# Performance work log

Hardware: AMD Instinct MI355X
Metric: run time of the kernel (lower is better)

## Reference

```python
import jax, jax.numpy as jnp
import numpy as np

NEG_SLOPE = 0.2  # LeakyReLU slope used by default activation_attn


def setup_inputs() -> dict:
    key = jax.random.key(0)
    k1, k2, k3, k4, k5 = jax.random.split(key, 5)
    N, K, F, H, D = 50000, 16, 128, 8, 64
    s = 1.0 / np.sqrt(F)  # roughly torch Linear init scale
    return {
        "x_self": jax.random.normal(k1, (N, F), dtype=jnp.float32),
        "x_neigh": jax.random.normal(k2, (N, K, F), dtype=jnp.float32),
        "W": jax.random.normal(k3, (H, F, D), dtype=jnp.float32) * s,
        "a_self": jax.random.normal(k4, (H, F), dtype=jnp.float32) * s,
        "a_neigh": jax.random.normal(k5, (H, F), dtype=jnp.float32) * s,
    }


def reference(x_self, x_neigh, W, a_self, a_neigh):
    # x_self: [N, F], x_neigh: [N, K, F]
    # x_all = concat(self, neigh) along neighbor axis -> [N, K+1, F]
    x_all = jnp.concatenate([x_self[:, None, :], x_neigh], axis=1)
    # per-head attention logits (each head's fc_attn_* is Linear(F, 1), no bias)
    logit_self = jnp.einsum('nf,hf->nh', x_self, a_self)          # [N, H]
    logit_all = jnp.einsum('nkf,hf->nkh', x_all, a_neigh)         # [N, K+1, H]
    logits = logit_self[:, None, :] + logit_all                   # [N, K+1, H]
    logits = jnp.where(logits >= 0, logits, NEG_SLOPE * logits)   # LeakyReLU(0.2)
    attn = jax.nn.softmax(logits, axis=1)                         # softmax over neighbors
    # per-head projection of all nodes: Linear(F, D), no bias
    xw = jnp.einsum('nkf,hfd->nkhd', x_all, W)                    # [N, K+1, H, D]
    h = jnp.einsum('nkhd,nkh->nhd', xw, attn)                     # [N, H, D]
    N, H, D = h.shape
    # concat aggregation: heads stacked along feature dim (head 0 first)
    return h.reshape(N, H * D)
```

## Files before the change

### kernel.cpp

```cpp
#include <hip/hip_runtime.h>

#define NTHREADS 256
#define NB 4
#define K 16
#define KP1 17
#define F 128
#define H 8
#define D 64
#define FP 132
#define NEG_SLOPE 0.2f


__global__ __launch_bounds__(NTHREADS, 4) void gat_kernel(
    const float* __restrict__ x_self,
    const float* __restrict__ x_neigh,
    const float* __restrict__ W,
    const float* __restrict__ a_self,
    const float* __restrict__ a_neigh,
    float* __restrict__ out,
    int N)
{
    __shared__ __align__(16) float xall[NB][KP1][FP];
    __shared__ __align__(16) float attn[NB][KP1][H];
    __shared__ float self_s[NB][H];

    float* yb = (float*)xall;

    const int tid = threadIdx.x;
    const int node0 = blockIdx.x * NB;

    {
        const int tot_self = NB * (F / 4);
        for (int i = tid; i < tot_self; i += NTHREADS) {
            int nb = i / (F / 4);
            int f4 = i % (F / 4);
            if (node0 + nb < N) {
                float4 v = ((const float4*)(x_self + (size_t)(node0 + nb) * F))[f4];
                *(float4*)&xall[nb][0][f4 * 4] = v;
            }
        }
        const int tot_n = NB * K * (F / 4);
        for (int i = tid; i < tot_n; i += NTHREADS) {
            int nb  = i / (K * F / 4);
            int rem = i % (K * F / 4);
            int k   = rem / (F / 4);
            int f4  = rem % (F / 4);
            if (node0 + nb < N) {
                float4 v = ((const float4*)(x_neigh + ((size_t)(node0 + nb) * K + k) * F))[f4];
                *(float4*)&xall[nb][k + 1][f4 * 4] = v;
            }
        }
    }
    __syncthreads();

    {
        const int p  = tid & 7;
        const int h  = (tid >> 3) & 7;
        const int nb = tid >> 6;
        const float* av  = a_neigh + h * F;
        const float* xr0 = &xall[nb][2 * p][0];
        const float* xr1 = &xall[nb][2 * p + 1][0];
        float4 s0 = {0.f, 0.f, 0.f, 0.f}, s1 = s0;
        #pragma unroll 8
        for (int f4 = 0; f4 < F / 4; f4++) {
            float4 avv = ((const float4*)av)[f4];
            float4 x0 = *(const float4*)(xr0 + f4 * 4);
            float4 x1 = *(const float4*)(xr1 + f4 * 4);
            s0.x += x0.x * avv.x; s0.y += x0.y * avv.y;
            s0.z += x0.z * avv.z; s0.w += x0.w * avv.w;
            s1.x += x1.x * avv.x; s1.y += x1.y * avv.y;
            s1.z += x1.z * avv.z; s1.w += x1.w * avv.w;
        }
        attn[nb][2 * p][h]     = (s0.x + s0.y) + (s0.z + s0.w);
        attn[nb][2 * p + 1][h] = (s1.x + s1.y) + (s1.z + s1.w);

        if (tid < 32) {
            const int h2  = tid & 7;
            const int nb2 = tid >> 3;
            const float* avn = a_neigh + h2 * F;
            const float* avs = a_self  + h2 * F;
            const float* x16 = &xall[nb2][16][0];
            const float* xs  = &xall[nb2][0][0];
            float4 t0 = {0.f, 0.f, 0.f, 0.f}, t1 = t0;
            #pragma unroll 8
            for (int f4 = 0; f4 < F / 4; f4++) {
                float4 an = ((const float4*)avn)[f4];
                float4 as = ((const float4*)avs)[f4];
                float4 v0 = *(const float4*)(x16 + f4 * 4);
                float4 v1 = *(const float4*)(xs  + f4 * 4);
                t0.x += v0.x * an.x; t0.y += v0.y * an.y;
                t0.z += v0.z * an.z; t0.w += v0.w * an.w;
                t1.x += v1.x * as.x; t1.y += v1.y * as.y;
                t1.z += v1.z * as.z; t1.w += v1.w * as.w;
            }
            attn[nb2][16][h2] = (t0.x + t0.y) + (t0.z + t0.w);
            self_s[nb2][h2]   = (t1.x + t1.y) + (t1.z + t1.w);
        }
    }
    __syncthreads();

    for (int i = tid; i < NB * H; i += NTHREADS) {
        int nb = i >> 3, h = i & 7;
        float sl = self_s[nb][h];
        float m = -1e30f;
        #pragma unroll
        for (int k = 0; k < KP1; k++) {
            float lg = sl + attn[nb][k][h];
            lg = (lg >= 0.f) ? lg : NEG_SLOPE * lg;
            attn[nb][k][h] = lg;
            m = fmaxf(m, lg);
        }
        float s = 0.f;
        #pragma unroll
        for (int k = 0; k < KP1; k++) {
            float e = __expf(attn[nb][k][h] - m);
            attn[nb][k][h] = e;
            s += e;
        }
        float inv = 1.0f / s;
        #pragma unroll
        for (int k = 0; k < KP1; k++) attn[nb][k][h] *= inv;
    }
    __syncthreads();

    {
        const int h  = (tid >> 5) & 7;
        const int f4 = tid & 31;
        float4 acc[NB];
        #pragma unroll
        for (int j = 0; j < NB; j++) acc[j] = {0.f, 0.f, 0.f, 0.f};
        for (int k = 0; k < KP1; k++) {
            #pragma unroll
            for (int j = 0; j < NB; j++) {
                float a = attn[j][k][h];
                float4 xv = *(const float4*)&xall[j][k][f4 * 4];
                acc[j].x += a * xv.x; acc[j].y += a * xv.y;
                acc[j].z += a * xv.z; acc[j].w += a * xv.w;
            }
        }
        __syncthreads();
        #pragma unroll
        for (int j = 0; j < NB; j++) {
            *(float4*)&yb[((size_t)j * H + h) * F + f4 * 4] = acc[j];
        }
    }
    __syncthreads();

    {
        const int lane = tid & 63;
        const int w    = tid >> 6;
        const int fg   = lane >> 4;
        const int d4   = lane & 15;
        const int h0 = w, h1 = w + 4;
        const float* Wb0 = W + ((size_t)h0 * F) * D + d4 * 4;
        const float* Wb1 = W + ((size_t)h1 * F) * D + d4 * 4;

        float4 acc0[NB], acc1[NB];
        #pragma unroll
        for (int nb = 0; nb < NB; nb++) {
            acc0[nb] = {0.f, 0.f, 0.f, 0.f};
            acc1[nb] = {0.f, 0.f, 0.f, 0.f};
        }

        for (int fb = 0; fb < 8; fb++) {
            const int f0 = fb * 16 + fg * 4;
            float4 w0[4], w1[4];
            #pragma unroll
            for (int ff = 0; ff < 4; ff++) {
                w0[ff] = *(const float4*)(Wb0 + (size_t)(f0 + ff) * D);
                w1[ff] = *(const float4*)(Wb1 + (size_t)(f0 + ff) * D);
            }
            float4 y0[NB], y1[NB];
            #pragma unroll
            for (int nb = 0; nb < NB; nb++) {
                y0[nb] = *(const float4*)&yb[((size_t)nb * H + h0) * F + f0];
                y1[nb] = *(const float4*)&yb[((size_t)nb * H + h1) * F + f0];
            }
            #pragma unroll
            for (int nb = 0; nb < NB; nb++) {
                acc0[nb].x += y0[nb].x * w0[0].x + y0[nb].y * w0[1].x + y0[nb].z * w0[2].x + y0[nb].w * w0[3].x;
                acc0[nb].y += y0[nb].x * w0[0].y + y0[nb].y * w0[1].y + y0[nb].z * w0[2].y + y0[nb].w * w0[3].y;
                acc0[nb].z += y0[nb].x * w0[0].z + y0[nb].y * w0[1].z + y0[nb].z * w0[2].z + y0[nb].w * w0[3].z;
                acc0[nb].w += y0[nb].x * w0[0].w + y0[nb].y * w0[1].w + y0[nb].z * w0[2].w + y0[nb].w * w0[3].w;
                acc1[nb].x += y1[nb].x * w1[0].x + y1[nb].y * w1[1].x + y1[nb].z * w1[2].x + y1[nb].w * w1[3].x;
                acc1[nb].y += y1[nb].x * w1[0].y + y1[nb].y * w1[1].y + y1[nb].z * w1[2].y + y1[nb].w * w1[3].y;
                acc1[nb].z += y1[nb].x * w1[0].z + y1[nb].y * w1[1].z + y1[nb].z * w1[2].z + y1[nb].w * w1[3].z;
                acc1[nb].w += y1[nb].x * w1[0].w + y1[nb].y * w1[1].w + y1[nb].z * w1[2].w + y1[nb].w * w1[3].w;
            }
        }

        #pragma unroll
        for (int nb = 0; nb < NB; nb++) {
            acc0[nb].x += __shfl_xor(acc0[nb].x, 16); acc0[nb].x += __shfl_xor(acc0[nb].x, 32);
            acc0[nb].y += __shfl_xor(acc0[nb].y, 16); acc0[nb].y += __shfl_xor(acc0[nb].y, 32);
            acc0[nb].z += __shfl_xor(acc0[nb].z, 16); acc0[nb].z += __shfl_xor(acc0[nb].z, 32);
            acc0[nb].w += __shfl_xor(acc0[nb].w, 16); acc0[nb].w += __shfl_xor(acc0[nb].w, 32);
            acc1[nb].x += __shfl_xor(acc1[nb].x, 16); acc1[nb].x += __shfl_xor(acc1[nb].x, 32);
            acc1[nb].y += __shfl_xor(acc1[nb].y, 16); acc1[nb].y += __shfl_xor(acc1[nb].y, 32);
            acc1[nb].z += __shfl_xor(acc1[nb].z, 16); acc1[nb].z += __shfl_xor(acc1[nb].z, 32);
            acc1[nb].w += __shfl_xor(acc1[nb].w, 16); acc1[nb].w += __shfl_xor(acc1[nb].w, 32);
        }

        #pragma unroll
        for (int nb = 0; nb < NB; nb++) {
            if (fg == nb && node0 + nb < N) {
                *(float4*)&out[(size_t)(node0 + nb) * (H * D) + h0 * D + d4 * 4] = acc0[nb];
                *(float4*)&out[(size_t)(node0 + nb) * (H * D) + h1 * D + d4 * 4] = acc1[nb];
            }
        }
    }
}

extern "C" void kernel_launch(void* const* d_in, const int* in_sizes, int n_in,
                              void* d_out, int out_size, void* d_ws, size_t ws_size,
                              hipStream_t stream) {
    const float* x_self  = (const float*)d_in[0];
    const float* x_neigh = (const float*)d_in[1];
    const float* W       = (const float*)d_in[2];
    const float* a_self  = (const float*)d_in[3];
    const float* a_neigh = (const float*)d_in[4];
    float* out = (float*)d_out;

    const int N = in_sizes[0] / F;
    const int nblocks = (N + NB - 1) / NB;
    gat_kernel<<<nblocks, NTHREADS, 0, stream>>>(x_self, x_neigh, W, a_self, a_neigh, out, N);
}
```

Measured before the change: 782.6 us.

## Transpose attention scratch, vectorize softmax/aggregation reads, prefetch W tiles

Transposes the shared attention buffer to [node][head][k] with padding so the logits, softmax and aggregation stages can use float4 loads and keep the logits in registers. The aggregation loop is unrolled in groups of four neighbors. The W projection loop now prefetches the next slice of W into registers while computing on the current one, to hide global load latency. The trade-off is more register pressure, which could reduce occupancy, plus a redundant wrap-around prefetch on the final iteration.

```diff
diff --git a/kernel.cpp b/kernel.cpp
--- a/kernel.cpp
+++ b/kernel.cpp
@@ -8,6 +8,7 @@
 #define H 8
 #define D 64
 #define FP 132
+#define ATP 20
 #define NEG_SLOPE 0.2f
 
 
@@ -21,7 +22,7 @@
     int N)
 {
     __shared__ __align__(16) float xall[NB][KP1][FP];
-    __shared__ __align__(16) float attn[NB][KP1][H];
+    __shared__ __align__(16) float attnT[NB][H][ATP];
     __shared__ float self_s[NB][H];
 
     float* yb = (float*)xall;
@@ -71,8 +72,9 @@
             s1.x += x1.x * avv.x; s1.y += x1.y * avv.y;
             s1.z += x1.z * avv.z; s1.w += x1.w * avv.w;
         }
-        attn[nb][2 * p][h]     = (s0.x + s0.y) + (s0.z + s0.w);
-        attn[nb][2 * p + 1][h] = (s1.x + s1.y) + (s1.z + s1.w);
+        float2 dots = { (s0.x + s0.y) + (s0.z + s0.w),
+                        (s1.x + s1.y) + (s1.z + s1.w) };
+        *(float2*)&attnT[nb][h][2 * p] = dots;
 
         if (tid < 32) {
             const int h2  = tid & 7;
@@ -93,8 +95,8 @@
                 t1.x += v1.x * as.x; t1.y += v1.y * as.y;
                 t1.z += v1.z * as.z; t1.w += v1.w * as.w;
             }
-            attn[nb2][16][h2] = (t0.x + t0.y) + (t0.z + t0.w);
-            self_s[nb2][h2]   = (t1.x + t1.y) + (t1.z + t1.w);
+            attnT[nb2][h2][16] = (t0.x + t0.y) + (t0.z + t0.w);
+            self_s[nb2][h2]    = (t1.x + t1.y) + (t1.z + t1.w);
         }
     }
     __syncthreads();
@@ -102,24 +104,42 @@
     for (int i = tid; i < NB * H; i += NTHREADS) {
         int nb = i >> 3, h = i & 7;
         float sl = self_s[nb][h];
-        float m = -1e30f;
-        #pragma unroll
-        for (int k = 0; k < KP1; k++) {
-            float lg = sl + attn[nb][k][h];
-            lg = (lg >= 0.f) ? lg : NEG_SLOPE * lg;
-            attn[nb][k][h] = lg;
-            m = fmaxf(m, lg);
-        }
+        float4 l0 = *(float4*)&attnT[nb][h][0];
+        float4 l1 = *(float4*)&attnT[nb][h][4];
+        float4 l2 = *(float4*)&attnT[nb][h][8];
+        float4 l3 = *(float4*)&attnT[nb][h][12];
+        float  l4 = attnT[nb][h][16];
+        #define LRELU(v) { v += sl; v = (v >= 0.f) ? v : NEG_SLOPE * v; }
+        LRELU(l0.x) LRELU(l0.y) LRELU(l0.z) LRELU(l0.w)
+        LRELU(l1.x) LRELU(l1.y) LRELU(l1.z) LRELU(l1.w)
+        LRELU(l2.x) LRELU(l2.y) LRELU(l2.z) LRELU(l2.w)
+        LRELU(l3.x) LRELU(l3.y) LRELU(l3.z) LRELU(l3.w)
+        LRELU(l4)
+        #undef LRELU
+        float m01 = fmaxf(fmaxf(fmaxf(l0.x, l0.y), fmaxf(l0.z, l0.w)),
+                          fmaxf(fmaxf(l1.x, l1.y), fmaxf(l1.z, l1.w)));
+        float m23 = fmaxf(fmaxf(fmaxf(l2.x, l2.y), fmaxf(l2.z, l2.w)),
+                          fmaxf(fmaxf(l3.x, l3.y), fmaxf(l3.z, l3.w)));
+        float m = fmaxf(fmaxf(m01, m23), l4);
         float s = 0.f;
-        #pragma unroll
-        for (int k = 0; k < KP1; k++) {
-            float e = __expf(attn[nb][k][h] - m);
-            attn[nb][k][h] = e;
-            s += e;
-        }
+        #define EXPS(v) { v = __expf(v - m); s += v; }
+        EXPS(l0.x) EXPS(l0.y) EXPS(l0.z) EXPS(l0.w)
+        EXPS(l1.x) EXPS(l1.y) EXPS(l1.z) EXPS(l1.w)
+        EXPS(l2.x) EXPS(l2.y) EXPS(l2.z) EXPS(l2.w)
+        EXPS(l3.x) EXPS(l3.y) EXPS(l3.z) EXPS(l3.w)
+        EXPS(l4)
+        #undef EXPS
         float inv = 1.0f / s;
-        #pragma unroll
-        for (int k = 0; k < KP1; k++) attn[nb][k][h] *= inv;
+        l0.x *= inv; l0.y *= inv; l0.z *= inv; l0.w *= inv;
+        l1.x *= inv; l1.y *= inv; l1.z *= inv; l1.w *= inv;
+        l2.x *= inv; l2.y *= inv; l2.z *= inv; l2.w *= inv;
+        l3.x *= inv; l3.y *= inv; l3.z *= inv; l3.w *= inv;
+        l4 *= inv;
+        *(float4*)&attnT[nb][h][0]  = l0;
+        *(float4*)&attnT[nb][h][4]  = l1;
+        *(float4*)&attnT[nb][h][8]  = l2;
+        *(float4*)&attnT[nb][h][12] = l3;
+        attnT[nb][h][16] = l4;
     }
     __syncthreads();
 
@@ -129,14 +149,29 @@
         float4 acc[NB];
         #pragma unroll
         for (int j = 0; j < NB; j++) acc[j] = {0.f, 0.f, 0.f, 0.f};
-        for (int k = 0; k < KP1; k++) {
+        #pragma unroll
+        for (int kq = 0; kq < 4; kq++) {
+            float4 a[NB];
+            #pragma unroll
+            for (int j = 0; j < NB; j++) a[j] = *(const float4*)&attnT[j][h][kq * 4];
             #pragma unroll
             for (int j = 0; j < NB; j++) {
-                float a = attn[j][k][h];
-                float4 xv = *(const float4*)&xall[j][k][f4 * 4];
-                acc[j].x += a * xv.x; acc[j].y += a * xv.y;
-                acc[j].z += a * xv.z; acc[j].w += a * xv.w;
-            }
+                float4 x0 = *(const float4*)&xall[j][kq * 4 + 0][f4 * 4];
+                float4 x1 = *(const float4*)&xall[j][kq * 4 + 1][f4 * 4];
+                float4 x2 = *(const float4*)&xall[j][kq * 4 + 2][f4 * 4];
+                float4 x3 = *(const float4*)&xall[j][kq * 4 + 3][f4 * 4];
+                acc[j].x += a[j].x * x0.x + a[j].y * x1.x + a[j].z * x2.x + a[j].w * x3.x;
+                acc[j].y += a[j].x * x0.y + a[j].y * x1.y + a[j].z * x2.y + a[j].w * x3.y;
+                acc[j].z += a[j].x * x0.z + a[j].y * x1.z + a[j].z * x2.z + a[j].w * x3.z;
+                acc[j].w += a[j].x * x0.w + a[j].y * x1.w + a[j].z * x2.w + a[j].w * x3.w;
+            }
+        }
+        #pragma unroll
+        for (int j = 0; j < NB; j++) {
+            float a16 = attnT[j][h][16];
+            float4 xv = *(const float4*)&xall[j][16][f4 * 4];
+            acc[j].x += a16 * xv.x; acc[j].y += a16 * xv.y;
+            acc[j].z += a16 * xv.z; acc[j].w += a16 * xv.w;
         }
         __syncthreads();
         #pragma unroll
@@ -162,31 +197,43 @@
             acc1[nb] = {0.f, 0.f, 0.f, 0.f};
         }
 
+        float4 c00 = *(const float4*)(Wb0 + (size_t)(fg * 4 + 0) * D);
+        float4 c01 = *(const float4*)(Wb0 + (size_t)(fg * 4 + 1) * D);
+        float4 c02 = *(const float4*)(Wb0 + (size_t)(fg * 4 + 2) * D);
+        float4 c03 = *(const float4*)(Wb0 + (size_t)(fg * 4 + 3) * D);
+        float4 c10 = *(const float4*)(Wb1 + (size_t)(fg * 4 + 0) * D);
+        float4 c11 = *(const float4*)(Wb1 + (size_t)(fg * 4 + 1) * D);
+        float4 c12 = *(const float4*)(Wb1 + (size_t)(fg * 4 + 2) * D);
+        float4 c13 = *(const float4*)(Wb1 + (size_t)(fg * 4 + 3) * D);
+
+        #pragma unroll
         for (int fb = 0; fb < 8; fb++) {
+            const int f0n = ((fb + 1) & 7) * 16 + fg * 4;
+            float4 n00 = *(const float4*)(Wb0 + (size_t)(f0n + 0) * D);
+            float4 n01 = *(const float4*)(Wb0 + (size_t)(f0n + 1) * D);
+            float4 n02 = *(const float4*)(Wb0 + (size_t)(f0n + 2) * D);
+            float4 n03 = *(const float4*)(Wb0 + (size_t)(f0n + 3) * D);
+            float4 n10 = *(const float4*)(Wb1 + (size_t)(f0n + 0) * D);
+            float4 n11 = *(const float4*)(Wb1 + (size_t)(f0n + 1) * D);
+            float4 n12 = *(const float4*)(Wb1 + (size_t)(f0n + 2) * D);
+            float4 n13 = *(const float4*)(Wb1 + (size_t)(f0n + 3) * D);
+
             const int f0 = fb * 16 + fg * 4;
-            float4 w0[4], w1[4];
-            #pragma unroll
-            for (int ff = 0; ff < 4; ff++) {
-                w0[ff] = *(const float4*)(Wb0 + (size_t)(f0 + ff) * D);
-                w1[ff] = *(const float4*)(Wb1 + (size_t)(f0 + ff) * D);
-            }
-            float4 y0[NB], y1[NB];
             #pragma unroll
             for (int nb = 0; nb < NB; nb++) {
-                y0[nb] = *(const float4*)&yb[((size_t)nb * H + h0) * F + f0];
-                y1[nb] = *(const float4*)&yb[((size_t)nb * H + h1) * F + f0];
-            }
-            #pragma unroll
-            for (int nb = 0; nb < NB; nb++) {
-                acc0[nb].x += y0[nb].x * w0[0].x + y0[nb].y * w0[1].x + y0[nb].z * w0[2].x + y0[nb].w * w0[3].x;
-                acc0[nb].y += y0[nb].x * w0[0].y + y0[nb].y * w0[1].y + y0[nb].z * w0[2].y + y0[nb].w * w0[3].y;
-                acc0[nb].z += y0[nb].x * w0[0].z + y0[nb].y * w0[1].z + y0[nb].z * w0[2].z + y0[nb].w * w0[3].z;
-                acc0[nb].w += y0[nb].x * w0[0].w + y0[nb].y * w0[1].w + y0[nb].z * w0[2].w + y0[nb].w * w0[3].w;
-                acc1[nb].x += y1[nb].x * w1[0].x + y1[nb].y * w1[1].x + y1[nb].z * w1[2].x + y1[nb].w * w1[3].x;
-                acc1[nb].y += y1[nb].x * w1[0].y + y1[nb].y * w1[1].y + y1[nb].z * w1[2].y + y1[nb].w * w1[3].y;
-                acc1[nb].z += y1[nb].x * w1[0].z + y1[nb].y * w1[1].z + y1[nb].z * w1[2].z + y1[nb].w * w1[3].z;
-                acc1[nb].w += y1[nb].x * w1[0].w + y1[nb].y * w1[1].w + y1[nb].z * w1[2].w + y1[nb].w * w1[3].w;
-            }
+                float4 y0 = *(const float4*)&yb[((size_t)nb * H + h0) * F + f0];
+                float4 y1 = *(const float4*)&yb[((size_t)nb * H + h1) * F + f0];
+                acc0[nb].x += y0.x * c00.x + y0.y * c01.x + y0.z * c02.x + y0.w * c03.x;
+                acc0[nb].y += y0.x * c00.y + y0.y * c01.y + y0.z * c02.y + y0.w * c03.y;
+                acc0[nb].z += y0.x * c00.z + y0.y * c01.z + y0.z * c02.z + y0.w * c03.z;
+                acc0[nb].w += y0.x * c00.w + y0.y * c01.w + y0.z * c02.w + y0.w * c03.w;
+                acc1[nb].x += y1.x * c10.x + y1.y * c11.x + y1.z * c12.x + y1.w * c13.x;
+                acc1[nb].y += y1.x * c10.y + y1.y * c11.y + y1.z * c12.y + y1.w * c13.y;
+                acc1[nb].z += y1.x * c10.z + y1.y * c11.z + y1.z * c12.z + y1.w * c13.z;
+                acc1[nb].w += y1.x * c10.w + y1.y * c11.w + y1.z * c12.w + y1.w * c13.w;
+            }
+            c00 = n00; c01 = n01; c02 = n02; c03 = n03;
+            c10 = n10; c11 = n11; c12 = n12; c13 = n13;
         }
 
         #pragma unroll
```

Result: slower. 1.436 ms (+83.5%).
